# Optimization experiments

Measured on AMD Instinct MI355X. Metric: run time of the kernel, lower is better.

Reference implementation:

```python
import jax, jax.numpy as jnp
import numpy as np

E = 8
HID = 2048
INTER = 1408
TOT = 8192


def setup_inputs() -> dict:
    key = jax.random.key(0)
    k1, k2, k3, k4, k5 = jax.random.split(key, 5)
    # uneven token counts per expert that sum exactly to TOT (grouped-GEMM ragged sizes)
    deltas = np.array([512, -256, 128, -384, 256, -512, 384, -128], dtype=np.int32)
    tokens_per_expert = jnp.asarray(TOT // E + deltas, dtype=jnp.int32)  # sums to TOT
    permuted_x = jax.random.normal(k1, (TOT, HID), dtype=jnp.float32)
    permuted_probs = jax.random.uniform(k2, (TOT,), dtype=jnp.float32)
    s_in = 1.0 / np.sqrt(HID)
    s_mid = 1.0 / np.sqrt(INTER)
    w_gate = jax.random.normal(k3, (E, HID, INTER), dtype=jnp.float32) * s_in
    w_up = jax.random.normal(k4, (E, HID, INTER), dtype=jnp.float32) * s_in
    w_down = jax.random.normal(k5, (E, INTER, HID), dtype=jnp.float32) * s_mid
    return {
        "permuted_x": permuted_x,
        "permuted_probs": permuted_probs,
        "w_gate": w_gate,
        "w_up": w_up,
        "w_down": w_down,
        "tokens_per_expert": tokens_per_expert,
    }


def reference(permuted_x, permuted_probs, w_gate, w_up, w_down, tokens_per_expert):
    # Grouped GEMM: tokens sorted by expert; lax.ragged_dot contracts each
    # contiguous group of rows against its expert's weight without padding.
    gate = jax.lax.ragged_dot(permuted_x, w_gate, tokens_per_expert)  # [T, INTER]
    up = jax.lax.ragged_dot(permuted_x, w_up, tokens_per_expert)      # [T, INTER]
    h = jax.nn.silu(gate) * up                                         # fused SiLU-mul
    values = jax.lax.ragged_dot(h, w_down, tokens_per_expert)          # [T, HID]
    return permuted_probs[:, None].astype(values.dtype) * values
```

## Files before the change

kernel.cpp:

```cpp
#include <hip/hip_runtime.h>

typedef unsigned short u16;
typedef unsigned int u32;
typedef u16 us8 __attribute__((ext_vector_type(8)));
typedef __bf16 bf16x8 __attribute__((ext_vector_type(8)));
typedef float f32x4 __attribute__((ext_vector_type(4)));

constexpr int kE = 8;
constexpr int kHID = 2048;
constexpr int kINTER = 1408;
constexpr int kTOT = 8192;

static __device__ __forceinline__ u16 f2bf(float f) {
  u32 u = __float_as_uint(f);
  u32 r = (u + 0x7fffu + ((u >> 16) & 1u)) >> 16;
  return (u16)r;
}

static __device__ __forceinline__ void gll16(const u16* g, u16* l) {
  __builtin_amdgcn_global_load_lds(
      (const __attribute__((address_space(1))) u32*)g,
      (__attribute__((address_space(3))) u32*)l, 16, 0, 0);
}

__global__ void conv_bf16(const float* __restrict__ x, u16* __restrict__ o) {
  size_t i = ((size_t)blockIdx.x * 256 + threadIdx.x) * 8;
  const float4* p = (const float4*)(x + i);
  float4 f0 = p[0], f1 = p[1];
  us8 v;
  v[0] = f2bf(f0.x); v[1] = f2bf(f0.y); v[2] = f2bf(f0.z); v[3] = f2bf(f0.w);
  v[4] = f2bf(f1.x); v[5] = f2bf(f1.y); v[6] = f2bf(f1.z); v[7] = f2bf(f1.w);
  *(us8*)(o + i) = v;
}

__global__ void transp_bf16(const float* __restrict__ w, u16* __restrict__ wt,
                            int K, int N) {
  __shared__ float tile[64][65];
  int e = blockIdx.z;
  const float* we = w + (size_t)e * K * N;
  u16* wte = wt + (size_t)e * K * N;
  int n0 = blockIdx.x * 64, k0 = blockIdx.y * 64;
  int t = threadIdx.x;
  int kl = t >> 4, n4 = (t & 15) * 4;
#pragma unroll
  for (int r = 0; r < 4; r++) {
    int k = r * 16 + kl;
    float4 v = *(const float4*)(we + (size_t)(k0 + k) * N + n0 + n4);
    tile[k][n4 + 0] = v.x; tile[k][n4 + 1] = v.y;
    tile[k][n4 + 2] = v.z; tile[k][n4 + 3] = v.w;
  }
  __syncthreads();
#pragma unroll
  for (int r = 0; r < 2; r++) {
    int c = r * 256 + t;
    int n = c >> 3, kc = (c & 7) * 8;
    us8 o;
#pragma unroll
    for (int j = 0; j < 8; j++) o[j] = f2bf(tile[kc + j][n]);
    *(us8*)(wte + (size_t)(n0 + n) * K + k0 + kc) = o;
  }
}

static __device__ __forceinline__ bool expert_of_tile(
    const int* __restrict__ tpe, int ty, int& e, int& m0, int& m_end) {
  int tile_base = 0, row_base = 0;
  e = -1;
  for (int i = 0; i < kE; i++) {
    int tc = tpe[i];
    int nt = (tc + 127) >> 7;
    if (e < 0 && ty < tile_base + nt) {
      e = i;
      m0 = row_base + (ty - tile_base) * 128;
      m_end = row_base + tc;
    }
    tile_base += nt;
    row_base += tc;
  }
  return e >= 0;
}

__launch_bounds__(256, 2)
__global__ void gemm1(const u16* __restrict__ Xb, const u16* __restrict__ Wgt,
                      const u16* __restrict__ Wut, const float* __restrict__ probs,
                      const int* __restrict__ tpe, u16* __restrict__ H) {
  __shared__ __align__(16) u16 As[128 * 32];
  __shared__ __align__(16) u16 Bgs[128 * 32];
  __shared__ __align__(16) u16 Bus[128 * 32];

  int e, m0, m_end;
  if (!expert_of_tile(tpe, blockIdx.y, e, m0, m_end)) return;
  int n0 = blockIdx.x * 128;

  int t = threadIdx.x;
  int w = t >> 6, lane = t & 63;
  int quad = lane >> 4, l15 = lane & 15;
  int wm = (w >> 1) * 64, wn = (w & 1) * 64;

  int ar0 = m0 + (t >> 2);      if (ar0 > kTOT - 1) ar0 = kTOT - 1;
  int ar1 = m0 + 64 + (t >> 2); if (ar1 > kTOT - 1) ar1 = kTOT - 1;
  const u16* gA0 = Xb + (size_t)ar0 * kHID + (t & 3) * 8;
  const u16* gA1 = Xb + (size_t)ar1 * kHID + (t & 3) * 8;
  size_t wbase = ((size_t)e * kINTER + n0 + (t >> 2)) * kHID + (t & 3) * 8;
  const u16* gBg0 = Wgt + wbase;
  const u16* gBg1 = gBg0 + (size_t)64 * kHID;
  const u16* gBu0 = Wut + wbase;
  const u16* gBu1 = gBu0 + (size_t)64 * kHID;
  u16* lA0 = As + (size_t)(w * 64) * 8;
  u16* lA1 = As + (size_t)(256 + w * 64) * 8;
  u16* lBg0 = Bgs + (size_t)(w * 64) * 8;
  u16* lBg1 = Bgs + (size_t)(256 + w * 64) * 8;
  u16* lBu0 = Bus + (size_t)(w * 64) * 8;
  u16* lBu1 = Bus + (size_t)(256 + w * 64) * 8;

  int aoff[4], boff[4];
#pragma unroll
  for (int i = 0; i < 4; i++) aoff[i] = (wm + i * 16 + l15) * 32 + quad * 8;
#pragma unroll
  for (int j = 0; j < 4; j++) boff[j] = (wn + j * 16 + l15) * 32 + quad * 8;

  f32x4 accg[4][4] = {};
  f32x4 accu[4][4] = {};

  for (int kt = 0; kt < kHID / 32; kt++) {
    gll16(gA0, lA0);  gll16(gA1, lA1);
    gll16(gBg0, lBg0); gll16(gBg1, lBg1);
    gll16(gBu0, lBu0); gll16(gBu1, lBu1);
    gA0 += 32; gA1 += 32; gBg0 += 32; gBg1 += 32; gBu0 += 32; gBu1 += 32;
    __syncthreads();

    bf16x8 a[4], bg[4], bu[4];
#pragma unroll
    for (int i = 0; i < 4; i++) a[i] = *(const bf16x8*)(As + aoff[i]);
#pragma unroll
    for (int j = 0; j < 4; j++) {
      bg[j] = *(const bf16x8*)(Bgs + boff[j]);
      bu[j] = *(const bf16x8*)(Bus + boff[j]);
    }
#pragma unroll
    for (int i = 0; i < 4; i++)
#pragma unroll
      for (int j = 0; j < 4; j++) {
        accg[i][j] = __builtin_amdgcn_mfma_f32_16x16x32_bf16(a[i], bg[j], accg[i][j], 0, 0, 0);
        accu[i][j] = __builtin_amdgcn_mfma_f32_16x16x32_bf16(a[i], bu[j], accu[i][j], 0, 0, 0);
      }
    __syncthreads();
  }

#pragma unroll
  for (int i = 0; i < 4; i++) {
#pragma unroll
    for (int r = 0; r < 4; r++) {
      int row = m0 + wm + i * 16 + quad * 4 + r;
      if (row < m_end) {
        float p = probs[row];
#pragma unroll
        for (int j = 0; j < 4; j++) {
          int col = n0 + wn + j * 16 + l15;
          float g = accg[i][j][r], u = accu[i][j][r];
          float s = g / (1.0f + __expf(-g));
          H[(size_t)row * kINTER + col] = f2bf(s * u * p);
        }
      }
    }
  }
}

__launch_bounds__(256, 2)
__global__ void gemm2(const u16* __restrict__ H, const u16* __restrict__ Wdt,
                      const int* __restrict__ tpe, float* __restrict__ out) {
  __shared__ __align__(16) u16 As[128 * 32];
  __shared__ __align__(16) u16 Bs[128 * 32];

  int e, m0, m_end;
  if (!expert_of_tile(tpe, blockIdx.y, e, m0, m_end)) return;
  int n0 = blockIdx.x * 128;

  int t = threadIdx.x;
  int w = t >> 6, lane = t & 63;
  int quad = lane >> 4, l15 = lane & 15;
  int wm = (w >> 1) * 64, wn = (w & 1) * 64;

  int ar0 = m0 + (t >> 2);      if (ar0 > kTOT - 1) ar0 = kTOT - 1;
  int ar1 = m0 + 64 + (t >> 2); if (ar1 > kTOT - 1) ar1 = kTOT - 1;
  const u16* gA0 = H + (size_t)ar0 * kINTER + (t & 3) * 8;
  const u16* gA1 = H + (size_t)ar1 * kINTER + (t & 3) * 8;
  const u16* gB0 = Wdt + ((size_t)e * kHID + n0 + (t >> 2)) * kINTER + (t & 3) * 8;
  const u16* gB1 = gB0 + (size_t)64 * kINTER;
  u16* lA0 = As + (size_t)(w * 64) * 8;
  u16* lA1 = As + (size_t)(256 + w * 64) * 8;
  u16* lB0 = Bs + (size_t)(w * 64) * 8;
  u16* lB1 = Bs + (size_t)(256 + w * 64) * 8;

  int aoff[4], boff[4];
#pragma unroll
  for (int i = 0; i < 4; i++) aoff[i] = (wm + i * 16 + l15) * 32 + quad * 8;
#pragma unroll
  for (int j = 0; j < 4; j++) boff[j] = (wn + j * 16 + l15) * 32 + quad * 8;

  f32x4 acc[4][4] = {};

  for (int kt = 0; kt < kINTER / 32; kt++) {
    gll16(gA0, lA0); gll16(gA1, lA1);
    gll16(gB0, lB0); gll16(gB1, lB1);
    gA0 += 32; gA1 += 32; gB0 += 32; gB1 += 32;
    __syncthreads();

    bf16x8 a[4], b[4];
#pragma unroll
    for (int i = 0; i < 4; i++) a[i] = *(const bf16x8*)(As + aoff[i]);
#pragma unroll
    for (int j = 0; j < 4; j++) b[j] = *(const bf16x8*)(Bs + boff[j]);
#pragma unroll
    for (int i = 0; i < 4; i++)
#pragma unroll
      for (int j = 0; j < 4; j++)
        acc[i][j] = __builtin_amdgcn_mfma_f32_16x16x32_bf16(a[i], b[j], acc[i][j], 0, 0, 0);
    __syncthreads();
  }

#pragma unroll
  for (int i = 0; i < 4; i++) {
#pragma unroll
    for (int r = 0; r < 4; r++) {
      int row = m0 + wm + i * 16 + quad * 4 + r;
      if (row < m_end) {
#pragma unroll
        for (int j = 0; j < 4; j++) {
          int col = n0 + wn + j * 16 + l15;
          out[(size_t)row * kHID + col] = acc[i][j][r];
        }
      }
    }
  }
}

extern "C" void kernel_launch(void* const* d_in, const int* in_sizes, int n_in,
                              void* d_out, int out_size, void* d_ws, size_t ws_size,
                              hipStream_t stream) {
  const float* x = (const float*)d_in[0];
  const float* probs = (const float*)d_in[1];
  const float* wg = (const float*)d_in[2];
  const float* wu = (const float*)d_in[3];
  const float* wd = (const float*)d_in[4];
  const int* tpe = (const int*)d_in[5];
  float* out = (float*)d_out;

  u16* ws = (u16*)d_ws;
  u16* Xb = ws;
  u16* Wgt = Xb + (size_t)kTOT * kHID;
  u16* Wut = Wgt + (size_t)kE * kINTER * kHID;
  u16* Wdt = Wut + (size_t)kE * kINTER * kHID;
  u16* H = Wdt + (size_t)kE * kHID * kINTER;

  conv_bf16<<<(kTOT * kHID) / (256 * 8), 256, 0, stream>>>(x, Xb);
  transp_bf16<<<dim3(kINTER / 64, kHID / 64, kE), 256, 0, stream>>>(wg, Wgt, kHID, kINTER);
  transp_bf16<<<dim3(kINTER / 64, kHID / 64, kE), 256, 0, stream>>>(wu, Wut, kHID, kINTER);
  transp_bf16<<<dim3(kHID / 64, kINTER / 64, kE), 256, 0, stream>>>(wd, Wdt, kINTER, kHID);

  gemm1<<<dim3(kINTER / 128, 72), 256, 0, stream>>>(Xb, Wgt, Wut, probs, tpe, H);
  gemm2<<<dim3(kHID / 128, 72), 256, 0, stream>>>(H, Wdt, tpe, out);
}
```

Before: 572.1 us.

## Enlarge grouped-GEMM tiles, double-buffer LDS, swizzle layout, and remap blocks across XCDs

Both grouped GEMMs move to 256-row expert tiles with 512-thread blocks; the down-projection also widens its tile to 256 columns. The K loop now uses 64-wide K slices with two LDS buffers, so global-to-LDS loads for the next slice overlap MFMA work on the current one. LDS rows are XOR-swizzled to cut bank conflicts. Blocks are remapped in groups with XCD awareness so neighbouring tiles share L2. The aim is more operand reuse per loaded byte and less load latency, at the cost of 128KB LDS per block, which lowers occupancy, and more padding waste on ragged expert tails.

Measured after the change: 535.5 us. 1.07x faster.

```diff
diff --git a/kernel.cpp b/kernel.cpp
--- a/kernel.cpp
+++ b/kernel.cpp
@@ -61,16 +61,16 @@
   }
 }
 
-static __device__ __forceinline__ bool expert_of_tile(
+static __device__ __forceinline__ bool expert_of_tile256(
     const int* __restrict__ tpe, int ty, int& e, int& m0, int& m_end) {
   int tile_base = 0, row_base = 0;
   e = -1;
   for (int i = 0; i < kE; i++) {
     int tc = tpe[i];
-    int nt = (tc + 127) >> 7;
+    int nt = (tc + 255) >> 8;
     if (e < 0 && ty < tile_base + nt) {
       e = i;
-      m0 = row_base + (ty - tile_base) * 128;
+      m0 = row_base + (ty - tile_base) * 256;
       m_end = row_base + tc;
     }
     tile_base += nt;
@@ -79,70 +79,106 @@
   return e >= 0;
 }
 
-__launch_bounds__(256, 2)
+static __device__ __forceinline__ void map_block(int& bx, int& by) {
+  int nx = gridDim.x, ny = gridDim.y;
+  int nwg = nx * ny;
+  int flat = blockIdx.y * nx + blockIdx.x;
+  int q = nwg >> 3, r = nwg & 7;
+  int xcd = flat & 7, lid = flat >> 3;
+  int nf = (xcd < r ? xcd * (q + 1) : r * (q + 1) + (xcd - r) * q) + lid;
+  const int G = 4;
+  int gs = G * nx;
+  int grp = nf / gs;
+  int wi = nf - grp * gs;
+  int rows = ny - grp * G;
+  if (rows > G) rows = G;
+  bx = wi / rows;
+  by = grp * G + (wi - bx * rows);
+}
+
+__launch_bounds__(512, 2)
 __global__ void gemm1(const u16* __restrict__ Xb, const u16* __restrict__ Wgt,
                       const u16* __restrict__ Wut, const float* __restrict__ probs,
                       const int* __restrict__ tpe, u16* __restrict__ H) {
-  __shared__ __align__(16) u16 As[128 * 32];
-  __shared__ __align__(16) u16 Bgs[128 * 32];
-  __shared__ __align__(16) u16 Bus[128 * 32];
-
+  __shared__ __align__(16) u16 sm[65536];
+  u16* A0 = sm;           u16* A1 = sm + 16384;
+  u16* Bg0 = sm + 32768;  u16* Bg1 = sm + 40960;
+  u16* Bu0 = sm + 49152;  u16* Bu1 = sm + 57344;
+
+  int bx, by; map_block(bx, by);
   int e, m0, m_end;
-  if (!expert_of_tile(tpe, blockIdx.y, e, m0, m_end)) return;
-  int n0 = blockIdx.x * 128;
+  if (!expert_of_tile256(tpe, by, e, m0, m_end)) return;
+  int n0 = bx * 128;
 
   int t = threadIdx.x;
   int w = t >> 6, lane = t & 63;
   int quad = lane >> 4, l15 = lane & 15;
   int wm = (w >> 1) * 64, wn = (w & 1) * 64;
 
-  int ar0 = m0 + (t >> 2);      if (ar0 > kTOT - 1) ar0 = kTOT - 1;
-  int ar1 = m0 + 64 + (t >> 2); if (ar1 > kTOT - 1) ar1 = kTOT - 1;
-  const u16* gA0 = Xb + (size_t)ar0 * kHID + (t & 3) * 8;
-  const u16* gA1 = Xb + (size_t)ar1 * kHID + (t & 3) * 8;
-  size_t wbase = ((size_t)e * kINTER + n0 + (t >> 2)) * kHID + (t & 3) * 8;
-  const u16* gBg0 = Wgt + wbase;
-  const u16* gBg1 = gBg0 + (size_t)64 * kHID;
-  const u16* gBu0 = Wut + wbase;
-  const u16* gBu1 = gBu0 + (size_t)64 * kHID;
-  u16* lA0 = As + (size_t)(w * 64) * 8;
-  u16* lA1 = As + (size_t)(256 + w * 64) * 8;
-  u16* lBg0 = Bgs + (size_t)(w * 64) * 8;
-  u16* lBg1 = Bgs + (size_t)(256 + w * 64) * 8;
-  u16* lBu0 = Bus + (size_t)(w * 64) * 8;
-  u16* lBu1 = Bus + (size_t)(256 + w * 64) * 8;
-
-  int aoff[4], boff[4];
-#pragma unroll
-  for (int i = 0; i < 4; i++) aoff[i] = (wm + i * 16 + l15) * 32 + quad * 8;
-#pragma unroll
-  for (int j = 0; j < 4; j++) boff[j] = (wn + j * 16 + l15) * 32 + quad * 8;
+  int trow = t >> 3;
+  int cg = (t & 7) ^ (trow & 7);
+  const u16* gA[4];
+#pragma unroll
+  for (int rr = 0; rr < 4; rr++) {
+    int row = m0 + rr * 64 + trow;
+    if (row > kTOT - 1) row = kTOT - 1;
+    gA[rr] = Xb + (size_t)row * kHID + cg * 8;
+  }
+  const u16 *gBg[2], *gBu[2];
+#pragma unroll
+  for (int rr = 0; rr < 2; rr++) {
+    size_t nrow = (size_t)e * kINTER + n0 + rr * 64 + trow;
+    gBg[rr] = Wgt + nrow * kHID + cg * 8;
+    gBu[rr] = Wut + nrow * kHID + cg * 8;
+  }
+
+  int abase = (wm + l15) * 64;
+  int bbase = (wn + l15) * 64;
+  int sz0 = ((quad ^ (l15 & 7)) << 3);
+  int sz1 = (((4 | quad) ^ (l15 & 7)) << 3);
 
   f32x4 accg[4][4] = {};
   f32x4 accu[4][4] = {};
 
-  for (int kt = 0; kt < kHID / 32; kt++) {
-    gll16(gA0, lA0);  gll16(gA1, lA1);
-    gll16(gBg0, lBg0); gll16(gBg1, lBg1);
-    gll16(gBu0, lBu0); gll16(gBu1, lBu1);
-    gA0 += 32; gA1 += 32; gBg0 += 32; gBg1 += 32; gBu0 += 32; gBu1 += 32;
+  auto stage = [&](u16* A, u16* Bg, u16* Bu, int ko) {
+#pragma unroll
+    for (int rr = 0; rr < 4; rr++) gll16(gA[rr] + ko, A + (rr * 64 + w * 8) * 64);
+#pragma unroll
+    for (int rr = 0; rr < 2; rr++) {
+      gll16(gBg[rr] + ko, Bg + (rr * 64 + w * 8) * 64);
+      gll16(gBu[rr] + ko, Bu + (rr * 64 + w * 8) * 64);
+    }
+  };
+  auto compute = [&](const u16* A, const u16* Bg, const u16* Bu) {
+#pragma unroll
+    for (int ks = 0; ks < 2; ks++) {
+      int sz = ks ? sz1 : sz0;
+      bf16x8 a[4], bg[4], bu[4];
+#pragma unroll
+      for (int i = 0; i < 4; i++) a[i] = *(const bf16x8*)(A + abase + i * 1024 + sz);
+#pragma unroll
+      for (int j = 0; j < 4; j++) {
+        bg[j] = *(const bf16x8*)(Bg + bbase + j * 1024 + sz);
+        bu[j] = *(const bf16x8*)(Bu + bbase + j * 1024 + sz);
+      }
+#pragma unroll
+      for (int i = 0; i < 4; i++)
+#pragma unroll
+        for (int j = 0; j < 4; j++) {
+          accg[i][j] = __builtin_amdgcn_mfma_f32_16x16x32_bf16(a[i], bg[j], accg[i][j], 0, 0, 0);
+          accu[i][j] = __builtin_amdgcn_mfma_f32_16x16x32_bf16(a[i], bu[j], accu[i][j], 0, 0, 0);
+        }
+    }
+  };
+
+  stage(A0, Bg0, Bu0, 0);
+  __syncthreads();
+  for (int kt = 0; kt < kHID / 64; kt += 2) {
+    stage(A1, Bg1, Bu1, (kt + 1) * 64);
+    compute(A0, Bg0, Bu0);
     __syncthreads();
-
-    bf16x8 a[4], bg[4], bu[4];
-#pragma unroll
-    for (int i = 0; i < 4; i++) a[i] = *(const bf16x8*)(As + aoff[i]);
-#pragma unroll
-    for (int j = 0; j < 4; j++) {
-      bg[j] = *(const bf16x8*)(Bgs + boff[j]);
-      bu[j] = *(const bf16x8*)(Bus + boff[j]);
-    }
-#pragma unroll
-    for (int i = 0; i < 4; i++)
-#pragma unroll
-      for (int j = 0; j < 4; j++) {
-        accg[i][j] = __builtin_amdgcn_mfma_f32_16x16x32_bf16(a[i], bg[j], accg[i][j], 0, 0, 0);
-        accu[i][j] = __builtin_amdgcn_mfma_f32_16x16x32_bf16(a[i], bu[j], accu[i][j], 0, 0, 0);
-      }
+    if (kt + 2 < kHID / 64) stage(A0, Bg0, Bu0, (kt + 2) * 64);
+    compute(A1, Bg1, Bu1);
     __syncthreads();
   }
 
@@ -165,61 +201,82 @@
   }
 }
 
-__launch_bounds__(256, 2)
+__launch_bounds__(512, 2)
 __global__ void gemm2(const u16* __restrict__ H, const u16* __restrict__ Wdt,
                       const int* __restrict__ tpe, float* __restrict__ out) {
-  __shared__ __align__(16) u16 As[128 * 32];
-  __shared__ __align__(16) u16 Bs[128 * 32];
-
+  __shared__ __align__(16) u16 sm[65536];
+  u16* A0 = sm;          u16* A1 = sm + 16384;
+  u16* B0 = sm + 32768;  u16* B1 = sm + 49152;
+
+  int bx, by; map_block(bx, by);
   int e, m0, m_end;
-  if (!expert_of_tile(tpe, blockIdx.y, e, m0, m_end)) return;
-  int n0 = blockIdx.x * 128;
+  if (!expert_of_tile256(tpe, by, e, m0, m_end)) return;
+  int n0 = bx * 256;
 
   int t = threadIdx.x;
   int w = t >> 6, lane = t & 63;
   int quad = lane >> 4, l15 = lane & 15;
-  int wm = (w >> 1) * 64, wn = (w & 1) * 64;
-
-  int ar0 = m0 + (t >> 2);      if (ar0 > kTOT - 1) ar0 = kTOT - 1;
-  int ar1 = m0 + 64 + (t >> 2); if (ar1 > kTOT - 1) ar1 = kTOT - 1;
-  const u16* gA0 = H + (size_t)ar0 * kINTER + (t & 3) * 8;
-  const u16* gA1 = H + (size_t)ar1 * kINTER + (t & 3) * 8;
-  const u16* gB0 = Wdt + ((size_t)e * kHID + n0 + (t >> 2)) * kINTER + (t & 3) * 8;
-  const u16* gB1 = gB0 + (size_t)64 * kINTER;
-  u16* lA0 = As + (size_t)(w * 64) * 8;
-  u16* lA1 = As + (size_t)(256 + w * 64) * 8;
-  u16* lB0 = Bs + (size_t)(w * 64) * 8;
-  u16* lB1 = Bs + (size_t)(256 + w * 64) * 8;
-
-  int aoff[4], boff[4];
-#pragma unroll
-  for (int i = 0; i < 4; i++) aoff[i] = (wm + i * 16 + l15) * 32 + quad * 8;
-#pragma unroll
-  for (int j = 0; j < 4; j++) boff[j] = (wn + j * 16 + l15) * 32 + quad * 8;
-
-  f32x4 acc[4][4] = {};
-
-  for (int kt = 0; kt < kINTER / 32; kt++) {
-    gll16(gA0, lA0); gll16(gA1, lA1);
-    gll16(gB0, lB0); gll16(gB1, lB1);
-    gA0 += 32; gA1 += 32; gB0 += 32; gB1 += 32;
+  int wm = (w >> 2) * 128, wn = (w & 3) * 64;
+
+  int trow = t >> 3;
+  int cg = (t & 7) ^ (trow & 7);
+  const u16* gA[4];
+#pragma unroll
+  for (int rr = 0; rr < 4; rr++) {
+    int row = m0 + rr * 64 + trow;
+    if (row > kTOT - 1) row = kTOT - 1;
+    gA[rr] = H + (size_t)row * kINTER + cg * 8;
+  }
+  const u16* gB[4];
+#pragma unroll
+  for (int rr = 0; rr < 4; rr++) {
+    size_t nrow = (size_t)e * kHID + n0 + rr * 64 + trow;
+    gB[rr] = Wdt + nrow * kINTER + cg * 8;
+  }
+
+  int abase = (wm + l15) * 64;
+  int bbase = (wn + l15) * 64;
+  int sz0 = ((quad ^ (l15 & 7)) << 3);
+  int sz1 = (((4 | quad) ^ (l15 & 7)) << 3);
+
+  f32x4 acc[8][4] = {};
+
+  auto stage = [&](u16* A, u16* B, int ko) {
+#pragma unroll
+    for (int rr = 0; rr < 4; rr++) gll16(gA[rr] + ko, A + (rr * 64 + w * 8) * 64);
+#pragma unroll
+    for (int rr = 0; rr < 4; rr++) gll16(gB[rr] + ko, B + (rr * 64 + w * 8) * 64);
+  };
+  auto compute = [&](const u16* A, const u16* B) {
+#pragma unroll
+    for (int ks = 0; ks < 2; ks++) {
+      int sz = ks ? sz1 : sz0;
+      bf16x8 a[8], b[4];
+#pragma unroll
+      for (int i = 0; i < 8; i++) a[i] = *(const bf16x8*)(A + abase + i * 1024 + sz);
+#pragma unroll
+      for (int j = 0; j < 4; j++) b[j] = *(const bf16x8*)(B + bbase + j * 1024 + sz);
+#pragma unroll
+      for (int i = 0; i < 8; i++)
+#pragma unroll
+        for (int j = 0; j < 4; j++)
+          acc[i][j] = __builtin_amdgcn_mfma_f32_16x16x32_bf16(a[i], b[j], acc[i][j], 0, 0, 0);
+    }
+  };
+
+  stage(A0, B0, 0);
+  __syncthreads();
+  for (int kt = 0; kt < kINTER / 64; kt += 2) {
+    stage(A1, B1, (kt + 1) * 64);
+    compute(A0, B0);
     __syncthreads();
-
-    bf16x8 a[4], b[4];
-#pragma unroll
-    for (int i = 0; i < 4; i++) a[i] = *(const bf16x8*)(As + aoff[i]);
-#pragma unroll
-    for (int j = 0; j < 4; j++) b[j] = *(const bf16x8*)(Bs + boff[j]);
-#pragma unroll
-    for (int i = 0; i < 4; i++)
-#pragma unroll
-      for (int j = 0; j < 4; j++)
-        acc[i][j] = __builtin_amdgcn_mfma_f32_16x16x32_bf16(a[i], b[j], acc[i][j], 0, 0, 0);
+    if (kt + 2 < kINTER / 64) stage(A0, B0, (kt + 2) * 64);
+    compute(A1, B1);
     __syncthreads();
   }
 
 #pragma unroll
-  for (int i = 0; i < 4; i++) {
+  for (int i = 0; i < 8; i++) {
 #pragma unroll
     for (int r = 0; r < 4; r++) {
       int row = m0 + wm + i * 16 + quad * 4 + r;
@@ -257,6 +314,6 @@
   transp_bf16<<<dim3(kINTER / 64, kHID / 64, kE), 256, 0, stream>>>(wu, Wut, kHID, kINTER);
   transp_bf16<<<dim3(kHID / 64, kINTER / 64, kE), 256, 0, stream>>>(wd, Wdt, kINTER, kHID);
 
-  gemm1<<<dim3(kINTER / 128, 72), 256, 0, stream>>>(Xb, Wgt, Wut, probs, tpe, H);
-  gemm2<<<dim3(kHID / 128, 72), 256, 0, stream>>>(H, Wdt, tpe, out);
-}
+  gemm1<<<dim3(kINTER / 128, 39), 512, 0, stream>>>(Xb, Wgt, Wut, probs, tpe, H);
+  gemm2<<<dim3(kHID / 256, 39), 512, 0, stream>>>(H, Wdt, tpe, out);
+}
```
